# Kernel optimization log

Hardware: AMD Instinct MI355X
Metric: run time of the kernel (lower is better)

The kernel has to match this reference:

```python
import jax, jax.numpy as jnp
import numpy as np

B, M, C = 8, 8192, 256   # batch, seeds, seed feature dim
F = 128                  # vote feature dim
P, K = 256, 32           # proposals, samples per group
CA, NCLS = 256, 10       # aggregated feat dim, classes
RADIUS = 0.3


def _lin(x, w, b):
    # 1x1 conv == pointwise linear; w: (out, in)
    return jnp.einsum('...c,oc->...o', x, w) + b


def _bnrelu(x, s, t):
    # eval-mode BatchNorm folded to per-channel affine, then ReLU
    return jnp.maximum(x * s + t, 0.0)


def _fps(xyz, npoint):
    # farthest point sampling; deterministic start at index 0
    Bb, N, _ = xyz.shape
    bidx = jnp.arange(Bb)

    def step(carry, _):
        distance, farthest = carry
        centroid = xyz[bidx, farthest][:, None, :]          # (B,1,2)
        d = jnp.sum((xyz - centroid) ** 2, -1)              # (B,N)
        distance = jnp.minimum(distance, d)
        return (distance, jnp.argmax(distance, -1)), farthest

    init = (jnp.full((Bb, N), 1e10, xyz.dtype), jnp.zeros((Bb,), jnp.int32))
    _, idx = jax.lax.scan(step, init, None, length=npoint)
    return jnp.transpose(idx)                               # (B, npoint)


def _ball_query(xyz, new_xyz, radius, nsample):
    # squared-distance cdist (monotone in euclid dist, so same sort order)
    N = xyz.shape[1]
    d2 = (jnp.sum(new_xyz ** 2, -1)[:, :, None]
          + jnp.sum(xyz ** 2, -1)[:, None, :]
          - 2.0 * jnp.einsum('bsd,bnd->bsn', new_xyz, xyz))  # (B,S,N)
    gidx = jnp.broadcast_to(jnp.arange(N), d2.shape)
    # out-of-radius points replaced by group_first (= index 0, as in source)
    gidx = jnp.where(d2 > radius * radius, 0, gidx)
    order = jnp.argsort(d2, axis=-1)
    return jnp.take_along_axis(gidx, order, axis=-1)[:, :, :nsample]


def _gather(points, idx):
    # points: (B,N,C); idx: (B,...) -> (B,...,C)
    return jax.vmap(lambda p, i: p[i])(points, idx)


def _forward(seed_xyz, seed_feats,
             v_off_w1, v_off_b1, v_off_s1, v_off_t1, v_off_w2, v_off_b2,
             v_ft_w1, v_ft_b1, v_ft_s1, v_ft_t1, v_ft_w2, v_ft_b2,
             a_w1, a_b1, a_s1, a_t1, a_w2, a_b2, a_s2, a_t2,
             p_w1, p_b1, p_s1, p_t1, p_w2, p_b2, p_s2, p_t2,
             obj_w, obj_b, cls_w, cls_b):
    # --- VotingModule (vote_factor=1) ---
    h = _bnrelu(_lin(seed_feats, v_off_w1, v_off_b1), v_off_s1, v_off_t1)
    offsets = _lin(h, v_off_w2, v_off_b2)                   # (B,M,2)
    g = _bnrelu(_lin(seed_feats, v_ft_w1, v_ft_b1), v_ft_s1, v_ft_t1)
    vote_feats = _lin(g, v_ft_w2, v_ft_b2)                  # (B,M,F)
    votes_xyz = seed_xyz + offsets                          # (B,M,2)

    # --- VoteAggregation ---
    fps_idx = _fps(votes_xyz, P)                            # (B,P)
    new_xyz = _gather(votes_xyz, fps_idx)                   # (B,P,2)
    gidx = _ball_query(votes_xyz, new_xyz, RADIUS, K)       # (B,P,K)
    gv = _gather(votes_xyz, gidx)                           # (B,P,K,2)
    gf = _gather(vote_feats, gidx)                          # (B,P,K,F)
    comb = jnp.concatenate([gv - new_xyz[:, :, None, :], gf], -1)  # (B,P,K,F+2)
    x = _bnrelu(_lin(comb, a_w1, a_b1), a_s1, a_t1)
    x = _bnrelu(_lin(x, a_w2, a_b2), a_s2, a_t2)
    pooled = jnp.max(x, axis=2)                             # (B,P,CA)

    # --- ProposalHead ---
    y = _bnrelu(_lin(pooled, p_w1, p_b1), p_s1, p_t1)
    y = _bnrelu(_lin(y, p_w2, p_b2), p_s2, p_t2)
    obj = _lin(y, obj_w, obj_b)[..., 0]                     # (B,P)
    cls = _lin(y, cls_w, cls_b)                             # (B,P,NCLS)
    return (new_xyz, obj, cls)


def setup_inputs() -> dict:
    key = jax.random.key(0)
    keys = iter(jax.random.split(key, 40))

    def w(shape):
        return (jax.random.normal(next(keys), shape) * 0.05).astype(jnp.float32)

    inp = {
        'seed_xyz': jax.random.uniform(next(keys), (B, M, 2), jnp.float32),
        'seed_feats': jax.random.normal(next(keys), (B, M, C), jnp.float32),
        # voting: offset branch
        'v_off_w1': w((C, C)), 'v_off_b1': w((C,)),
        'v_off_s1': 1.0 + w((C,)), 'v_off_t1': w((C,)),
        'v_off_w2': w((2, C)), 'v_off_b2': w((2,)),
        # voting: feature branch
        'v_ft_w1': w((C, C)), 'v_ft_b1': w((C,)),
        'v_ft_s1': 1.0 + w((C,)), 'v_ft_t1': w((C,)),
        'v_ft_w2': w((F, C)), 'v_ft_b2': w((F,)),
        # aggregation MLP
        'a_w1': w((CA, F + 2)), 'a_b1': w((CA,)),
        'a_s1': 1.0 + w((CA,)), 'a_t1': w((CA,)),
        'a_w2': w((CA, CA)), 'a_b2': w((CA,)),
        'a_s2': 1.0 + w((CA,)), 'a_t2': w((CA,)),
        # proposal head
        'p_w1': w((CA, CA)), 'p_b1': w((CA,)),
        'p_s1': 1.0 + w((CA,)), 'p_t1': w((CA,)),
        'p_w2': w((CA // 2, CA)), 'p_b2': w((CA // 2,)),
        'p_s2': 1.0 + w((CA // 2,)), 'p_t2': w((CA // 2,)),
        'obj_w': w((1, CA // 2)), 'obj_b': w((1,)),
        'cls_w': w((NCLS, CA // 2)), 'cls_b': w((NCLS,)),
    }
    return inp


def reference(seed_xyz, seed_feats,
              v_off_w1, v_off_b1, v_off_s1, v_off_t1, v_off_w2, v_off_b2,
              v_ft_w1, v_ft_b1, v_ft_s1, v_ft_t1, v_ft_w2, v_ft_b2,
              a_w1, a_b1, a_s1, a_t1, a_w2, a_b2, a_s2, a_t2,
              p_w1, p_b1, p_s1, p_t1, p_w2, p_b2, p_s2, p_t2,
              obj_w, obj_b, cls_w, cls_b):
    return _forward(seed_xyz, seed_feats,
                    v_off_w1, v_off_b1, v_off_s1, v_off_t1, v_off_w2, v_off_b2,
                    v_ft_w1, v_ft_b1, v_ft_s1, v_ft_t1, v_ft_w2, v_ft_b2,
                    a_w1, a_b1, a_s1, a_t1, a_w2, a_b2, a_s2, a_t2,
                    p_w1, p_b1, p_s1, p_t1, p_w2, p_b2, p_s2, p_t2,
                    obj_w, obj_b, cls_w, cls_b)
```

## Files before the change

### kernel.cpp

```cpp
#include <hip/hip_runtime.h>

typedef __attribute__((ext_vector_type(8))) short bf16x8;
typedef __attribute__((ext_vector_type(4))) float f32x4;
typedef unsigned short u16;
typedef unsigned int u32;
typedef unsigned long long u64;

#define DEV static __device__ __forceinline__
DEV u16 f2bf(float f) { u32 i = __float_as_uint(f); i += 0x7fffu + ((i >> 16) & 1u); return (u16)(i >> 16); }
DEV float bf2f(u16 u) { return __uint_as_float(((u32)u) << 16); }

constexpr int Mn = 8192;
constexpr int Pn = 256;
constexpr int Kn = 32;
constexpr float R2 = 0.09f;

__global__ __launch_bounds__(256, 2) void k_voting_off(
    const float* __restrict__ sxyz,
    const float* __restrict__ sfeat,
    const float* __restrict__ ow1, const float* __restrict__ ob1,
    const float* __restrict__ os1, const float* __restrict__ ot1,
    const float* __restrict__ ow2, const float* __restrict__ ob2,
    float* __restrict__ votes)
{
  __shared__ __align__(16) float Xc[16][34];
  __shared__ __align__(16) float Wc[16][262];
  __shared__ __align__(16) float Hst[256][33];

  const int tid = threadIdx.x;
  const int row0 = blockIdx.x * 32;

  const int wv = tid >> 6;
  const int w8 = wv * 8;
  const int cg = tid & 63;

  float acc[8][4];
#pragma unroll
  for (int r = 0; r < 8; ++r)
#pragma unroll
    for (int j = 0; j < 4; ++j) acc[r][j] = 0.f;

  for (int kc = 0; kc < 16; ++kc) {
    __syncthreads();
    for (int i = tid; i < 256 * 16; i += 256) {
      int o = i >> 4, k = i & 15;
      Wc[k][o] = ow1[o * 256 + kc * 16 + k];
    }
    for (int i = tid; i < 32 * 16; i += 256) {
      int r = i >> 4, k = i & 15;
      Xc[k][r] = sfeat[(row0 + r) * 256 + kc * 16 + k];
    }
    __syncthreads();
#pragma unroll
    for (int k = 0; k < 16; ++k) {
      float2 x01 = *(const float2*)&Xc[k][w8];
      float2 x23 = *(const float2*)&Xc[k][w8 + 2];
      float2 x45 = *(const float2*)&Xc[k][w8 + 4];
      float2 x67 = *(const float2*)&Xc[k][w8 + 6];
      float2 wlo = *(const float2*)&Wc[k][2 * cg];
      float2 whi = *(const float2*)&Wc[k][128 + 2 * cg];
      float x[8] = {x01.x, x01.y, x23.x, x23.y, x45.x, x45.y, x67.x, x67.y};
      float w[4] = {wlo.x, wlo.y, whi.x, whi.y};
#pragma unroll
      for (int r = 0; r < 8; ++r)
#pragma unroll
        for (int j = 0; j < 4; ++j)
          acc[r][j] = fmaf(x[r], w[j], acc[r][j]);
    }
  }
  __syncthreads();
#pragma unroll
  for (int j = 0; j < 4; ++j) {
    int o = (j < 2) ? (2 * cg + j) : (126 + 2 * cg + j);
    float bb = ob1[o], ss = os1[o], tt = ot1[o];
#pragma unroll
    for (int r = 0; r < 8; ++r)
      Hst[o][w8 + r] = fmaxf((acc[r][j] + bb) * ss + tt, 0.f);
  }
  __syncthreads();

  if (tid < 64) {
    int r = tid >> 1, o = tid & 1;
    float a = 0.f;
    for (int k = 0; k < 256; ++k)
      a = fmaf(Hst[k][r], ow2[o * 256 + k], a);
    a += ob2[o];
    int row = row0 + r;
    votes[row * 2 + o] = sxyz[row * 2 + o] + a;
  }
}

__global__ __launch_bounds__(512, 1) void k_fps(
    const float* __restrict__ votes, float* __restrict__ nxyz,
    float* __restrict__ out)
{
  const int b = blockIdx.x, tid = threadIdx.x;
  const float* vb = votes + b * Mn * 2;
  __shared__ float2 xy[Mn];
  __shared__ u32 Sd[2][32], Sl[2][32];
  __shared__ float histx[256], histy[256];

  {
    const float4* vb4 = (const float4*)vb;
#pragma unroll
    for (int j = tid; j < Mn / 2; j += 512) {
      float4 v = vb4[j];
      *(float4*)&xy[2 * j] = v;
    }
  }
  float dist[16];
#pragma unroll
  for (int s = 0; s < 16; ++s) dist[s] = 1e10f;
  __syncthreads();

  float cx = xy[0].x, cy = xy[0].y;
  if (tid == 0) { histx[0] = cx; histy[0] = cy; }

  for (int it = 1; it < Pn; ++it) {
    float bd = -1.f; int sb = 0;
#pragma unroll
    for (int s = 0; s < 16; ++s) {
      float2 p = xy[s * 512 + tid];
      float dx = p.x - cx, dy = p.y - cy;
      float d = fminf(dist[s], dx * dx + dy * dy);
      dist[s] = d;
      if (d > bd) { bd = d; sb = s; }
    }
    int bi = sb * 512 + tid;

    u32 hd = __float_as_uint(bd), hl = ~(u32)bi;

#define FPS_ROR(VD, VL, N)                                                      \
    {                                                                           \
      u32 od = (u32)__builtin_amdgcn_update_dpp(0, (int)VD, 0x120 + N, 0xF, 0xF, false); \
      u32 ol = (u32)__builtin_amdgcn_update_dpp(0, (int)VL, 0x120 + N, 0xF, 0xF, false); \
      bool g = (od > VD) || (od == VD && ol > VL);                              \
      VD = g ? od : VD; VL = g ? ol : VL;                                       \
    }
    FPS_ROR(hd, hl, 8)
    FPS_ROR(hd, hl, 4)
    FPS_ROR(hd, hl, 2)
    FPS_ROR(hd, hl, 1)

    const int buf = it & 1;
    if ((tid & 15) == 0) {
      int row = tid >> 4;
      Sd[buf][row] = hd; Sl[buf][row] = hl;
    }
    __syncthreads();

    int rr = tid & 15;
    u32 rd = Sd[buf][rr], rl = Sl[buf][rr];
    {
      u32 od = Sd[buf][16 + rr], ol = Sl[buf][16 + rr];
      bool g = (od > rd) || (od == rd && ol > rl);
      rd = g ? od : rd; rl = g ? ol : rl;
    }
    FPS_ROR(rd, rl, 8)
    FPS_ROR(rd, rl, 4)
    FPS_ROR(rd, rl, 2)
    FPS_ROR(rd, rl, 1)
#undef FPS_ROR

    int widx = (int)(~rl);
    float2 w = xy[widx];
    cx = w.x; cy = w.y;
    if (tid == 0) { histx[it] = cx; histy[it] = cy; }
  }
  __syncthreads();
  if (tid < 256) {
    float2 o2; o2.x = histx[tid]; o2.y = histy[tid];
    *(float2*)&nxyz[(b * Pn + tid) * 2] = o2;
    *(float2*)&out[(b * Pn + tid) * 2] = o2;
  }
}

__global__ __launch_bounds__(256) void k_ballq(
    const float* __restrict__ votes, const float* __restrict__ nxyz,
    int* __restrict__ gidx)
{
  const int bp = blockIdx.x, tid = threadIdx.x;
  const int b = bp >> 8;
  const float* vb = votes + b * Mn * 2;
  const float sx = nxyz[bp * 2], sy = nxyz[bp * 2 + 1];
  const float a = sx * sx + sy * sy;
  float d2[32];
#pragma unroll
  for (int s = 0; s < 32; ++s) {
    int i = tid * 32 + s;
    float x = vb[i * 2], y = vb[i * 2 + 1];
    d2[s] = (a + (x * x + y * y)) - 2.f * (sx * x + sy * y);
  }
  __shared__ float sd[4];
  __shared__ int si[4];
  __shared__ int swi;
  unsigned mask = 0;
  for (int kk = 0; kk < Kn; ++kk) {
    float bd = 3.4e38f; int bi = 0x7fffffff;
#pragma unroll
    for (int s = 0; s < 32; ++s)
      if (!((mask >> s) & 1u) && d2[s] < bd) { bd = d2[s]; bi = tid * 32 + s; }
#pragma unroll
    for (int off = 32; off > 0; off >>= 1) {
      float od = __shfl_xor(bd, off);
      int oi = __shfl_xor(bi, off);
      if (od < bd || (od == bd && oi < bi)) { bd = od; bi = oi; }
    }
    if ((tid & 63) == 0) { sd[tid >> 6] = bd; si[tid >> 6] = bi; }
    __syncthreads();
    if (tid == 0) {
#pragma unroll
      for (int w = 1; w < 4; ++w)
        if (sd[w] < bd || (sd[w] == bd && si[w] < bi)) { bd = sd[w]; bi = si[w]; }
      swi = bi;
      gidx[bp * Kn + kk] = (bd > R2) ? 0 : bi;
    }
    __syncthreads();
    int wi = swi;
    if ((wi >> 5) == tid) mask |= 1u << (wi & 31);
  }
}

__global__ __launch_bounds__(256) void k_prep(
    const float* __restrict__ fw1, const float* __restrict__ fw2,
    const float* __restrict__ aw1, const float* __restrict__ aw2,
    u16* __restrict__ FW1h, u16* __restrict__ FW2b,
    u16* __restrict__ AW1b, u16* __restrict__ AW2b)
{
  const int gid = blockIdx.x * 256 + threadIdx.x;
  const int gsz = gridDim.x * 256;
  for (int i = gid; i < 65536; i += gsz) FW1h[i] = f2bf(fw1[i]);
  for (int i = gid; i < 32768; i += gsz) FW2b[i] = f2bf(fw2[i]);
  for (int i = gid; i < 65536; i += gsz) AW2b[i] = f2bf(aw2[i]);
  for (int i = gid; i < 49152; i += gsz) {
    int o = i / 192, k = i % 192;
    AW1b[i] = (k < 130) ? f2bf(aw1[o * 130 + k]) : (u16)0;
  }
}

__global__ __launch_bounds__(256) void k_vf(
    const float* __restrict__ sfeat, const u16* __restrict__ FW1h,
    const float* __restrict__ fb1, const float* __restrict__ fs1,
    const float* __restrict__ ft1, const u16* __restrict__ FW2b,
    const float* __restrict__ fb2, u16* __restrict__ vfeat)
{
  __shared__ u16 Hs[128 * 136];
  __shared__ u16 As[128 * 40];
  __shared__ u16 Bs[128 * 40];
  const int tid = threadIdx.x;
  const int row0 = blockIdx.x * 128;
  const int wid = tid >> 6, lane = tid & 63, m16 = lane & 15, quad = lane >> 4;
  const int wr = wid >> 1, wc = wid & 1;
  const int sr = tid >> 1, sk = (tid & 1) * 16;

  f32x4 acc2[4][4];
#pragma unroll
  for (int mt = 0; mt < 4; ++mt)
#pragma unroll
    for (int nt = 0; nt < 4; ++nt) acc2[mt][nt] = (f32x4){0.f, 0.f, 0.f, 0.f};

  for (int h = 0; h < 2; ++h) {
    f32x4 acc[4][4];
#pragma unroll
    for (int mt = 0; mt < 4; ++mt)
#pragma unroll
      for (int nt = 0; nt < 4; ++nt) acc[mt][nt] = (f32x4){0.f, 0.f, 0.f, 0.f};

    for (int s = 0; s < 8; ++s) {
      __syncthreads();
      {
        const float* src = &sfeat[(row0 + sr) * 256 + s * 32 + sk];
        u32 packed[8];
#pragma unroll
        for (int q = 0; q < 4; ++q) {
          float4 v = *(const float4*)&src[q * 4];
          packed[q * 2]     = (u32)f2bf(v.x) | ((u32)f2bf(v.y) << 16);
          packed[q * 2 + 1] = (u32)f2bf(v.z) | ((u32)f2bf(v.w) << 16);
        }
        *(uint4*)&As[sr * 40 + sk]     = *(uint4*)&packed[0];
        *(uint4*)&As[sr * 40 + sk + 8] = *(uint4*)&packed[4];
        const u16* bsrc = &FW1h[(h * 128 + sr) * 256 + s * 32 + sk];
        *(uint4*)&Bs[sr * 40 + sk]     = *(const uint4*)&bsrc[0];
        *(uint4*)&Bs[sr * 40 + sk + 8] = *(const uint4*)&bsrc[8];
      }
      __syncthreads();
#pragma unroll
      for (int mt = 0; mt < 4; ++mt) {
        bf16x8 af = *(const bf16x8*)&As[(wr * 64 + mt * 16 + m16) * 40 + quad * 8];
#pragma unroll
        for (int nt = 0; nt < 4; ++nt) {
          bf16x8 bfr = *(const bf16x8*)&Bs[(wc * 64 + nt * 16 + m16) * 40 + quad * 8];
          acc[mt][nt] = __builtin_amdgcn_mfma_f32_16x16x32_bf16(af, bfr, acc[mt][nt], 0, 0, 0);
        }
      }
    }
    __syncthreads();
#pragma unroll
    for (int nt = 0; nt < 4; ++nt) {
      int colL = wc * 64 + nt * 16 + m16;
      int col = h * 128 + colL;
      float bb = fb1[col], ss = fs1[col], tt = ft1[col];
#pragma unroll
      for (int mt = 0; mt < 4; ++mt) {
        int rL = wr * 64 + mt * 16 + quad * 4;
#pragma unroll
        for (int r = 0; r < 4; ++r)
          Hs[(rL + r) * 136 + colL] = f2bf(fmaxf((acc[mt][nt][r] + bb) * ss + tt, 0.f));
      }
    }
    for (int s2 = 0; s2 < 4; ++s2) {
      __syncthreads();
      {
        const u16* bsrc = &FW2b[sr * 256 + h * 128 + s2 * 32 + sk];
        *(uint4*)&Bs[sr * 40 + sk]     = *(const uint4*)&bsrc[0];
        *(uint4*)&Bs[sr * 40 + sk + 8] = *(const uint4*)&bsrc[8];
      }
      __syncthreads();
#pragma unroll
      for (int mt = 0; mt < 4; ++mt) {
        bf16x8 af = *(const bf16x8*)&Hs[(wr * 64 + mt * 16 + m16) * 136 + s2 * 32 + quad * 8];
#pragma unroll
        for (int nt = 0; nt < 4; ++nt) {
          bf16x8 bfr = *(const bf16x8*)&Bs[(wc * 64 + nt * 16 + m16) * 40 + quad * 8];
          acc2[mt][nt] = __builtin_amdgcn_mfma_f32_16x16x32_bf16(af, bfr, acc2[mt][nt], 0, 0, 0);
        }
      }
    }
  }
#pragma unroll
  for (int nt = 0; nt < 4; ++nt) {
    int col = wc * 64 + nt * 16 + m16;
    float bb = fb2[col];
#pragma unroll
    for (int mt = 0; mt < 4; ++mt) {
      int rbase = row0 + wr * 64 + mt * 16 + quad * 4;
#pragma unroll
      for (int r = 0; r < 4; ++r)
        vfeat[(rbase + r) * 128 + col] = f2bf(acc2[mt][nt][r] + bb);
    }
  }
}

__global__ __launch_bounds__(256) void k_agg(
    const float* __restrict__ votes, const u16* __restrict__ vfeat,
    const float* __restrict__ nxyz, const int* __restrict__ gidx,
    const u16* __restrict__ AW1b, const float* __restrict__ ab1,
    const float* __restrict__ as1, const float* __restrict__ at1,
    const u16* __restrict__ AW2b, const float* __restrict__ ab2,
    const float* __restrict__ as2, const float* __restrict__ at2,
    float* __restrict__ pooled)
{
  __shared__ u16 U[32 * 264];
  __shared__ u16 Bs[256 * 72];
  __shared__ int gix[32];
  __shared__ float gvx[32], gvy[32];
  u16* CombA = U;
  u16* As = U;
  float* x2T = (float*)Bs;

  const int bp = blockIdx.x, tid = threadIdx.x, b = bp >> 8;
  if (tid < 32) {
    int g = gidx[bp * 32 + tid];
    gix[tid] = g;
    gvx[tid] = votes[(b * Mn + g) * 2];
    gvy[tid] = votes[(b * Mn + g) * 2 + 1];
  }
  __syncthreads();
  const float sx = nxyz[bp * 2], sy = nxyz[bp * 2 + 1];

  if (tid < 192) {
    int row = tid / 6, c = tid % 6;
    const u16* vsrc = &vfeat[(b * Mn + gix[row]) * 128];
    u16* dst = &CombA[row * 200 + c * 32];
    if (c == 0) {
      dst[0] = f2bf(gvx[row] - sx);
      dst[1] = f2bf(gvy[row] - sy);
      for (int k = 2; k < 32; ++k) dst[k] = vsrc[k - 2];
    } else if (c <= 3) {
      for (int k = 0; k < 32; ++k) dst[k] = vsrc[c * 32 + k - 2];
    } else if (c == 4) {
      dst[0] = vsrc[126]; dst[1] = vsrc[127];
      for (int k = 2; k < 32; ++k) dst[k] = 0;
    } else {
      for (int k = 0; k < 32; ++k) dst[k] = 0;
    }
  }

  const int wid = tid >> 6, lane = tid & 63, m16 = lane & 15, quad = lane >> 4;
  const int mt = wid & 1, nh = wid >> 1;

  f32x4 acc[8];
#pragma unroll
  for (int nt = 0; nt < 8; ++nt) acc[nt] = (f32x4){0.f, 0.f, 0.f, 0.f};
  for (int s = 0; s < 3; ++s) {
    __syncthreads();
    for (int i = tid; i < 4096; i += 256) {
      int n = i >> 4, c4 = i & 15;
      *(uint2*)&Bs[n * 72 + c4 * 4] = *(const uint2*)&AW1b[n * 192 + s * 64 + c4 * 4];
    }
    __syncthreads();
#pragma unroll
    for (int ks = 0; ks < 2; ++ks) {
      bf16x8 af = *(const bf16x8*)&CombA[(mt * 16 + m16) * 200 + s * 64 + ks * 32 + quad * 8];
#pragma unroll
      for (int nt = 0; nt < 8; ++nt) {
        bf16x8 bf_ = *(const bf16x8*)&Bs[(nh * 128 + nt * 16 + m16) * 72 + ks * 32 + quad * 8];
        acc[nt] = __builtin_amdgcn_mfma_f32_16x16x32_bf16(af, bf_, acc[nt], 0, 0, 0);
      }
    }
  }
  __syncthreads();
#pragma unroll
  for (int nt = 0; nt < 8; ++nt) {
    int col = nh * 128 + nt * 16 + m16;
    float bb = ab1[col], ss = as1[col], tt = at1[col];
#pragma unroll
    for (int r = 0; r < 4; ++r) {
      int samp = mt * 16 + quad * 4 + r;
      As[samp * 264 + col] = f2bf(fmaxf((acc[nt][r] + bb) * ss + tt, 0.f));
    }
  }

  f32x4 acc2[8];
#pragma unroll
  for (int nt = 0; nt < 8; ++nt) acc2[nt] = (f32x4){0.f, 0.f, 0.f, 0.f};
  for (int s = 0; s < 4; ++s) {
    __syncthreads();
    for (int i = tid; i < 4096; i += 256) {
      int n = i >> 4, c4 = i & 15;
      *(uint2*)&Bs[n * 72 + c4 * 4] = *(const uint2*)&AW2b[n * 256 + s * 64 + c4 * 4];
    }
    __syncthreads();
#pragma unroll
    for (int ks = 0; ks < 2; ++ks) {
      bf16x8 af = *(const bf16x8*)&As[(mt * 16 + m16) * 264 + s * 64 + ks * 32 + quad * 8];
#pragma unroll
      for (int nt = 0; nt < 8; ++nt) {
        bf16x8 bf_ = *(const bf16x8*)&Bs[(nh * 128 + nt * 16 + m16) * 72 + ks * 32 + quad * 8];
        acc2[nt] = __builtin_amdgcn_mfma_f32_16x16x32_bf16(af, bf_, acc2[nt], 0, 0, 0);
      }
    }
  }
  __syncthreads();
#pragma unroll
  for (int nt = 0; nt < 8; ++nt) {
    int col = nh * 128 + nt * 16 + m16;
    float bb = ab2[col], ss = as2[col], tt = at2[col];
#pragma unroll
    for (int r = 0; r < 4; ++r) {
      int samp = mt * 16 + quad * 4 + r;
      x2T[col * 33 + samp] = fmaxf((acc2[nt][r] + bb) * ss + tt, 0.f);
    }
  }
  __syncthreads();
  {
    float m = x2T[tid * 33];
#pragma unroll
    for (int s2 = 1; s2 < 32; ++s2) m = fmaxf(m, x2T[tid * 33 + s2]);
    pooled[bp * 256 + tid] = m;
  }
}

__global__ __launch_bounds__(256) void k_head(
    const float* __restrict__ pooled,
    const float* __restrict__ pw1, const float* __restrict__ pb1,
    const float* __restrict__ ps1, const float* __restrict__ pt1,
    const float* __restrict__ pw2, const float* __restrict__ pb2,
    const float* __restrict__ ps2, const float* __restrict__ pt2,
    const float* __restrict__ objw, const float* __restrict__ objb,
    const float* __restrict__ clsw, const float* __restrict__ clsb,
    float* __restrict__ out)
{
  __shared__ float xr[256], y1[256], y2[128];
  const int bp = blockIdx.x, tid = threadIdx.x;
  xr[tid] = pooled[bp * 256 + tid];
  __syncthreads();
  {
    float a = 0.f;
    for (int c = 0; c < 256; ++c) a = fmaf(xr[c], pw1[tid * 256 + c], a);
    a = (a + pb1[tid]) * ps1[tid] + pt1[tid];
    y1[tid] = fmaxf(a, 0.f);
  }
  __syncthreads();
  if (tid < 128) {
    float a = 0.f;
    for (int c = 0; c < 256; ++c) a = fmaf(y1[c], pw2[tid * 256 + c], a);
    a = (a + pb2[tid]) * ps2[tid] + pt2[tid];
    y2[tid] = fmaxf(a, 0.f);
  }
  __syncthreads();
  if (tid < 10) {
    float a = 0.f;
    for (int c = 0; c < 128; ++c) a = fmaf(y2[c], clsw[tid * 128 + c], a);
    out[6144 + bp * 10 + tid] = a + clsb[tid];
  } else if (tid == 10) {
    float a = 0.f;
    for (int c = 0; c < 128; ++c) a = fmaf(y2[c], objw[c], a);
    out[4096 + bp] = a + objb[0];
  }
}

extern "C" void kernel_launch(void* const* d_in, const int* in_sizes, int n_in,
                              void* d_out, int out_size, void* d_ws, size_t ws_size,
                              hipStream_t stream)
{
  (void)in_sizes; (void)n_in; (void)out_size; (void)ws_size;
  const float* sxyz  = (const float*)d_in[0];
  const float* sfeat = (const float*)d_in[1];
  const float* ow1 = (const float*)d_in[2];
  const float* ob1 = (const float*)d_in[3];
  const float* os1 = (const float*)d_in[4];
  const float* ot1 = (const float*)d_in[5];
  const float* ow2 = (const float*)d_in[6];
  const float* ob2 = (const float*)d_in[7];
  const float* fw1 = (const float*)d_in[8];
  const float* fb1 = (const float*)d_in[9];
  const float* fs1 = (const float*)d_in[10];
  const float* ft1 = (const float*)d_in[11];
  const float* fw2 = (const float*)d_in[12];
  const float* fb2 = (const float*)d_in[13];
  const float* aw1 = (const float*)d_in[14];
  const float* ab1 = (const float*)d_in[15];
  const float* as1 = (const float*)d_in[16];
  const float* at1 = (const float*)d_in[17];
  const float* aw2 = (const float*)d_in[18];
  const float* ab2 = (const float*)d_in[19];
  const float* as2 = (const float*)d_in[20];
  const float* at2 = (const float*)d_in[21];
  const float* pw1 = (const float*)d_in[22];
  const float* pb1 = (const float*)d_in[23];
  const float* ps1 = (const float*)d_in[24];
  const float* pt1 = (const float*)d_in[25];
  const float* pw2 = (const float*)d_in[26];
  const float* pb2 = (const float*)d_in[27];
  const float* ps2 = (const float*)d_in[28];
  const float* pt2 = (const float*)d_in[29];
  const float* objw = (const float*)d_in[30];
  const float* objb = (const float*)d_in[31];
  const float* clsw = (const float*)d_in[32];
  const float* clsb = (const float*)d_in[33];

  char* ws = (char*)d_ws;
  float* votes  = (float*)(ws + 0);
  u16*   vfeat  = (u16*)  (ws + 524288);
  float* nxyz   = (float*)(ws + 17301504);
  int*   gidxp  = (int*)  (ws + 17317888);
  float* pooled = (float*)(ws + 17580032);
  u16*   FW1h   = (u16*)  (ws + 19677184);
  u16*   FW2b   = (u16*)  (ws + 19808256);
  u16*   AW1b   = (u16*)  (ws + 19873792);
  u16*   AW2b   = (u16*)  (ws + 19972096);
  float* out    = (float*)d_out;

  k_voting_off<<<dim3(2048), dim3(256), 0, stream>>>(
      sxyz, sfeat, ow1, ob1, os1, ot1, ow2, ob2, votes);

  k_fps<<<dim3(8), dim3(512), 0, stream>>>(votes, nxyz, out);

  k_ballq<<<dim3(2048), dim3(256), 0, stream>>>(votes, nxyz, gidxp);

  k_prep<<<dim3(256), dim3(256), 0, stream>>>(
      fw1, fw2, aw1, aw2, FW1h, FW2b, AW1b, AW2b);

  k_vf<<<dim3(512), dim3(256), 0, stream>>>(
      sfeat, FW1h, fb1, fs1, ft1, FW2b, fb2, vfeat);

  k_agg<<<dim3(2048), dim3(256), 0, stream>>>(
      votes, vfeat, nxyz, gidxp, AW1b, ab1, as1, at1,
      AW2b, ab2, as2, at2, pooled);

  k_head<<<dim3(2048), dim3(256), 0, stream>>>(
      pooled, pw1, pb1, ps1, pt1, pw2, pb2, ps2, pt2,
      objw, objb, clsw, clsb, out);
}
```

Baseline: 938.2 us.

## Merge FPS and vote-feature MLP into one launch so they overlap

Combines the serial 8-block FPS kernel and the vote-feature GEMM kernel into a single 520-block launch. The first 8 blocks run FPS and the rest run the feature MLP, so the long latency-bound FPS runs alongside the GEMM work instead of leaving most CUs idle. The GEMM part is retiled for 512 threads (8 waves, 32 columns each), and k_prep is moved ahead so its weights are ready. Risks: the shared-memory union is 86 KB and the launch bound changes, which may limit occupancy for the GEMM blocks. The FPS blocks may also be scheduled after GEMM blocks, which would stretch the critical path.

```diff
diff --git a/kernel.cpp b/kernel.cpp
--- a/kernel.cpp
+++ b/kernel.cpp
@@ -90,88 +90,194 @@
   }
 }
 
-__global__ __launch_bounds__(512, 1) void k_fps(
+__global__ __launch_bounds__(512) void k_fps_vf(
     const float* __restrict__ votes, float* __restrict__ nxyz,
-    float* __restrict__ out)
-{
-  const int b = blockIdx.x, tid = threadIdx.x;
-  const float* vb = votes + b * Mn * 2;
-  __shared__ float2 xy[Mn];
-  __shared__ u32 Sd[2][32], Sl[2][32];
-  __shared__ float histx[256], histy[256];
-
-  {
-    const float4* vb4 = (const float4*)vb;
-#pragma unroll
-    for (int j = tid; j < Mn / 2; j += 512) {
-      float4 v = vb4[j];
-      *(float4*)&xy[2 * j] = v;
-    }
-  }
-  float dist[16];
-#pragma unroll
-  for (int s = 0; s < 16; ++s) dist[s] = 1e10f;
-  __syncthreads();
-
-  float cx = xy[0].x, cy = xy[0].y;
-  if (tid == 0) { histx[0] = cx; histy[0] = cy; }
-
-  for (int it = 1; it < Pn; ++it) {
-    float bd = -1.f; int sb = 0;
-#pragma unroll
-    for (int s = 0; s < 16; ++s) {
-      float2 p = xy[s * 512 + tid];
-      float dx = p.x - cx, dy = p.y - cy;
-      float d = fminf(dist[s], dx * dx + dy * dy);
-      dist[s] = d;
-      if (d > bd) { bd = d; sb = s; }
-    }
-    int bi = sb * 512 + tid;
-
-    u32 hd = __float_as_uint(bd), hl = ~(u32)bi;
+    float* __restrict__ out,
+    const float* __restrict__ sfeat, const u16* __restrict__ FW1h,
+    const float* __restrict__ fb1, const float* __restrict__ fs1,
+    const float* __restrict__ ft1, const u16* __restrict__ FW2b,
+    const float* __restrict__ fb2, u16* __restrict__ vfeat)
+{
+  __shared__ __align__(16) char smem[86016];
+  const int tid = threadIdx.x;
+
+  if (blockIdx.x < 8) {
+    const int b = blockIdx.x;
+    const float* vb = votes + b * Mn * 2;
+    float2* xy   = (float2*)smem;
+    u32*   Sd    = (u32*)(smem + 65536);
+    u32*   Sl    = (u32*)(smem + 65536 + 256);
+    float* histx = (float*)(smem + 66048);
+    float* histy = (float*)(smem + 67072);
+
+    {
+      const float4* vb4 = (const float4*)vb;
+#pragma unroll
+      for (int j = tid; j < Mn / 2; j += 512) {
+        float4 v = vb4[j];
+        *(float4*)&xy[2 * j] = v;
+      }
+    }
+    float dist[16];
+#pragma unroll
+    for (int s = 0; s < 16; ++s) dist[s] = 1e10f;
+    __syncthreads();
+
+    float cx = xy[0].x, cy = xy[0].y;
+    if (tid == 0) { histx[0] = cx; histy[0] = cy; }
+
+    for (int it = 1; it < Pn; ++it) {
+      float bd = -1.f; int sb = 0;
+#pragma unroll
+      for (int s = 0; s < 16; ++s) {
+        float2 p = xy[s * 512 + tid];
+        float dx = p.x - cx, dy = p.y - cy;
+        float d = fminf(dist[s], dx * dx + dy * dy);
+        dist[s] = d;
+        if (d > bd) { bd = d; sb = s; }
+      }
+      int bi = sb * 512 + tid;
+
+      u32 hd = __float_as_uint(bd), hl = ~(u32)bi;
 
 #define FPS_ROR(VD, VL, N)                                                      \
-    {                                                                           \
-      u32 od = (u32)__builtin_amdgcn_update_dpp(0, (int)VD, 0x120 + N, 0xF, 0xF, false); \
-      u32 ol = (u32)__builtin_amdgcn_update_dpp(0, (int)VL, 0x120 + N, 0xF, 0xF, false); \
-      bool g = (od > VD) || (od == VD && ol > VL);                              \
-      VD = g ? od : VD; VL = g ? ol : VL;                                       \
-    }
-    FPS_ROR(hd, hl, 8)
-    FPS_ROR(hd, hl, 4)
-    FPS_ROR(hd, hl, 2)
-    FPS_ROR(hd, hl, 1)
-
-    const int buf = it & 1;
-    if ((tid & 15) == 0) {
-      int row = tid >> 4;
-      Sd[buf][row] = hd; Sl[buf][row] = hl;
-    }
-    __syncthreads();
-
-    int rr = tid & 15;
-    u32 rd = Sd[buf][rr], rl = Sl[buf][rr];
-    {
-      u32 od = Sd[buf][16 + rr], ol = Sl[buf][16 + rr];
-      bool g = (od > rd) || (od == rd && ol > rl);
-      rd = g ? od : rd; rl = g ? ol : rl;
-    }
-    FPS_ROR(rd, rl, 8)
-    FPS_ROR(rd, rl, 4)
-    FPS_ROR(rd, rl, 2)
-    FPS_ROR(rd, rl, 1)
+      {                                                                         \
+        u32 od = (u32)__builtin_amdgcn_update_dpp(0, (int)VD, 0x120 + N, 0xF, 0xF, false); \
+        u32 ol = (u32)__builtin_amdgcn_update_dpp(0, (int)VL, 0x120 + N, 0xF, 0xF, false); \
+        bool g = (od > VD) || (od == VD && ol > VL);                            \
+        VD = g ? od : VD; VL = g ? ol : VL;                                     \
+      }
+      FPS_ROR(hd, hl, 8)
+      FPS_ROR(hd, hl, 4)
+      FPS_ROR(hd, hl, 2)
+      FPS_ROR(hd, hl, 1)
+
+      const int buf = it & 1;
+      if ((tid & 15) == 0) {
+        int row = tid >> 4;
+        Sd[buf * 32 + row] = hd; Sl[buf * 32 + row] = hl;
+      }
+      __syncthreads();
+
+      int rr = tid & 15;
+      u32 rd = Sd[buf * 32 + rr], rl = Sl[buf * 32 + rr];
+      {
+        u32 od = Sd[buf * 32 + 16 + rr], ol = Sl[buf * 32 + 16 + rr];
+        bool g = (od > rd) || (od == rd && ol > rl);
+        rd = g ? od : rd; rl = g ? ol : rl;
+      }
+      FPS_ROR(rd, rl, 8)
+      FPS_ROR(rd, rl, 4)
+      FPS_ROR(rd, rl, 2)
+      FPS_ROR(rd, rl, 1)
 #undef FPS_ROR
 
-    int widx = (int)(~rl);
-    float2 w = xy[widx];
-    cx = w.x; cy = w.y;
-    if (tid == 0) { histx[it] = cx; histy[it] = cy; }
-  }
-  __syncthreads();
-  if (tid < 256) {
-    float2 o2; o2.x = histx[tid]; o2.y = histy[tid];
-    *(float2*)&nxyz[(b * Pn + tid) * 2] = o2;
-    *(float2*)&out[(b * Pn + tid) * 2] = o2;
+      int widx = (int)(~rl);
+      float2 w = xy[widx];
+      cx = w.x; cy = w.y;
+      if (tid == 0) { histx[it] = cx; histy[it] = cy; }
+    }
+    __syncthreads();
+    if (tid < 256) {
+      float2 o2; o2.x = histx[tid]; o2.y = histy[tid];
+      *(float2*)&nxyz[(b * Pn + tid) * 2] = o2;
+      *(float2*)&out[(b * Pn + tid) * 2] = o2;
+    }
+  } else {
+    const int bx = blockIdx.x - 8;
+    const int row0 = bx * 128;
+    u16* Hs = (u16*)smem;
+    u16* As = (u16*)(smem + 34816);
+    u16* Bs = (u16*)(smem + 45056);
+
+    const int wid = tid >> 6, lane = tid & 63, m16 = lane & 15, quad = lane >> 4;
+    const int wr = wid >> 2;
+    const int wc4 = wid & 3;
+    const int sr = tid >> 2, sk = (tid & 3) * 8;
+
+    f32x4 acc2[4][2];
+#pragma unroll
+    for (int mt = 0; mt < 4; ++mt)
+#pragma unroll
+      for (int nt = 0; nt < 2; ++nt) acc2[mt][nt] = (f32x4){0.f, 0.f, 0.f, 0.f};
+
+    for (int h = 0; h < 2; ++h) {
+      f32x4 acc[4][2];
+#pragma unroll
+      for (int mt = 0; mt < 4; ++mt)
+#pragma unroll
+        for (int nt = 0; nt < 2; ++nt) acc[mt][nt] = (f32x4){0.f, 0.f, 0.f, 0.f};
+
+      for (int s = 0; s < 8; ++s) {
+        __syncthreads();
+        {
+          const float* src = &sfeat[(row0 + sr) * 256 + s * 32 + sk];
+          float4 v0 = *(const float4*)&src[0];
+          float4 v1 = *(const float4*)&src[4];
+          u32 packed[4];
+          packed[0] = (u32)f2bf(v0.x) | ((u32)f2bf(v0.y) << 16);
+          packed[1] = (u32)f2bf(v0.z) | ((u32)f2bf(v0.w) << 16);
+          packed[2] = (u32)f2bf(v1.x) | ((u32)f2bf(v1.y) << 16);
+          packed[3] = (u32)f2bf(v1.z) | ((u32)f2bf(v1.w) << 16);
+          *(uint4*)&As[sr * 40 + sk] = *(uint4*)&packed[0];
+          *(uint4*)&Bs[sr * 40 + sk] =
+              *(const uint4*)&FW1h[(h * 128 + sr) * 256 + s * 32 + sk];
+        }
+        __syncthreads();
+#pragma unroll
+        for (int mt = 0; mt < 4; ++mt) {
+          bf16x8 af = *(const bf16x8*)&As[(wr * 64 + mt * 16 + m16) * 40 + quad * 8];
+#pragma unroll
+          for (int nt = 0; nt < 2; ++nt) {
+            bf16x8 bfr = *(const bf16x8*)&Bs[(wc4 * 32 + nt * 16 + m16) * 40 + quad * 8];
+            acc[mt][nt] = __builtin_amdgcn_mfma_f32_16x16x32_bf16(af, bfr, acc[mt][nt], 0, 0, 0);
+          }
+        }
+      }
+      __syncthreads();
+#pragma unroll
+      for (int nt = 0; nt < 2; ++nt) {
+        int colL = wc4 * 32 + nt * 16 + m16;
+        int col = h * 128 + colL;
+        float bb = fb1[col], ss = fs1[col], tt = ft1[col];
+#pragma unroll
+        for (int mt = 0; mt < 4; ++mt) {
+          int rL = wr * 64 + mt * 16 + quad * 4;
+#pragma unroll
+          for (int r = 0; r < 4; ++r)
+            Hs[(rL + r) * 136 + colL] = f2bf(fmaxf((acc[mt][nt][r] + bb) * ss + tt, 0.f));
+        }
+      }
+      for (int s2 = 0; s2 < 4; ++s2) {
+        __syncthreads();
+        {
+          *(uint4*)&Bs[sr * 40 + sk] =
+              *(const uint4*)&FW2b[sr * 256 + h * 128 + s2 * 32 + sk];
+        }
+        __syncthreads();
+#pragma unroll
+        for (int mt = 0; mt < 4; ++mt) {
+          bf16x8 af = *(const bf16x8*)&Hs[(wr * 64 + mt * 16 + m16) * 136 + s2 * 32 + quad * 8];
+#pragma unroll
+          for (int nt = 0; nt < 2; ++nt) {
+            bf16x8 bfr = *(const bf16x8*)&Bs[(wc4 * 32 + nt * 16 + m16) * 40 + quad * 8];
+            acc2[mt][nt] = __builtin_amdgcn_mfma_f32_16x16x32_bf16(af, bfr, acc2[mt][nt], 0, 0, 0);
+          }
+        }
+      }
+    }
+#pragma unroll
+    for (int nt = 0; nt < 2; ++nt) {
+      int col = wc4 * 32 + nt * 16 + m16;
+      float bb = fb2[col];
+#pragma unroll
+      for (int mt = 0; mt < 4; ++mt) {
+        int rbase = row0 + wr * 64 + mt * 16 + quad * 4;
+#pragma unroll
+        for (int r = 0; r < 4; ++r)
+          vfeat[(rbase + r) * 128 + col] = f2bf(acc2[mt][nt][r] + bb);
+      }
+    }
   }
 }
 
@@ -235,109 +341,6 @@
   for (int i = gid; i < 49152; i += gsz) {
     int o = i / 192, k = i % 192;
     AW1b[i] = (k < 130) ? f2bf(aw1[o * 130 + k]) : (u16)0;
-  }
-}
-
-__global__ __launch_bounds__(256) void k_vf(
-    const float* __restrict__ sfeat, const u16* __restrict__ FW1h,
-    const float* __restrict__ fb1, const float* __restrict__ fs1,
-    const float* __restrict__ ft1, const u16* __restrict__ FW2b,
-    const float* __restrict__ fb2, u16* __restrict__ vfeat)
-{
-  __shared__ u16 Hs[128 * 136];
-  __shared__ u16 As[128 * 40];
-  __shared__ u16 Bs[128 * 40];
-  const int tid = threadIdx.x;
-  const int row0 = blockIdx.x * 128;
-  const int wid = tid >> 6, lane = tid & 63, m16 = lane & 15, quad = lane >> 4;
-  const int wr = wid >> 1, wc = wid & 1;
-  const int sr = tid >> 1, sk = (tid & 1) * 16;
-
-  f32x4 acc2[4][4];
-#pragma unroll
-  for (int mt = 0; mt < 4; ++mt)
-#pragma unroll
-    for (int nt = 0; nt < 4; ++nt) acc2[mt][nt] = (f32x4){0.f, 0.f, 0.f, 0.f};
-
-  for (int h = 0; h < 2; ++h) {
-    f32x4 acc[4][4];
-#pragma unroll
-    for (int mt = 0; mt < 4; ++mt)
-#pragma unroll
-      for (int nt = 0; nt < 4; ++nt) acc[mt][nt] = (f32x4){0.f, 0.f, 0.f, 0.f};
-
-    for (int s = 0; s < 8; ++s) {
-      __syncthreads();
-      {
-        const float* src = &sfeat[(row0 + sr) * 256 + s * 32 + sk];
-        u32 packed[8];
-#pragma unroll
-        for (int q = 0; q < 4; ++q) {
-          float4 v = *(const float4*)&src[q * 4];
-          packed[q * 2]     = (u32)f2bf(v.x) | ((u32)f2bf(v.y) << 16);
-          packed[q * 2 + 1] = (u32)f2bf(v.z) | ((u32)f2bf(v.w) << 16);
-        }
-        *(uint4*)&As[sr * 40 + sk]     = *(uint4*)&packed[0];
-        *(uint4*)&As[sr * 40 + sk + 8] = *(uint4*)&packed[4];
-        const u16* bsrc = &FW1h[(h * 128 + sr) * 256 + s * 32 + sk];
-        *(uint4*)&Bs[sr * 40 + sk]     = *(const uint4*)&bsrc[0];
-        *(uint4*)&Bs[sr * 40 + sk + 8] = *(const uint4*)&bsrc[8];
-      }
-      __syncthreads();
-#pragma unroll
-      for (int mt = 0; mt < 4; ++mt) {
-        bf16x8 af = *(const bf16x8*)&As[(wr * 64 + mt * 16 + m16) * 40 + quad * 8];
-#pragma unroll
-        for (int nt = 0; nt < 4; ++nt) {
-          bf16x8 bfr = *(const bf16x8*)&Bs[(wc * 64 + nt * 16 + m16) * 40 + quad * 8];
-          acc[mt][nt] = __builtin_amdgcn_mfma_f32_16x16x32_bf16(af, bfr, acc[mt][nt], 0, 0, 0);
-        }
-      }
-    }
-    __syncthreads();
-#pragma unroll
-    for (int nt = 0; nt < 4; ++nt) {
-      int colL = wc * 64 + nt * 16 + m16;
-      int col = h * 128 + colL;
-      float bb = fb1[col], ss = fs1[col], tt = ft1[col];
-#pragma unroll
-      for (int mt = 0; mt < 4; ++mt) {
-        int rL = wr * 64 + mt * 16 + quad * 4;
-#pragma unroll
-        for (int r = 0; r < 4; ++r)
-          Hs[(rL + r) * 136 + colL] = f2bf(fmaxf((acc[mt][nt][r] + bb) * ss + tt, 0.f));
-      }
-    }
-    for (int s2 = 0; s2 < 4; ++s2) {
-      __syncthreads();
-      {
-        const u16* bsrc = &FW2b[sr * 256 + h * 128 + s2 * 32 + sk];
-        *(uint4*)&Bs[sr * 40 + sk]     = *(const uint4*)&bsrc[0];
-        *(uint4*)&Bs[sr * 40 + sk + 8] = *(const uint4*)&bsrc[8];
-      }
-      __syncthreads();
-#pragma unroll
-      for (int mt = 0; mt < 4; ++mt) {
-        bf16x8 af = *(const bf16x8*)&Hs[(wr * 64 + mt * 16 + m16) * 136 + s2 * 32 + quad * 8];
-#pragma unroll
-        for (int nt = 0; nt < 4; ++nt) {
-          bf16x8 bfr = *(const bf16x8*)&Bs[(wc * 64 + nt * 16 + m16) * 40 + quad * 8];
-          acc2[mt][nt] = __builtin_amdgcn_mfma_f32_16x16x32_bf16(af, bfr, acc2[mt][nt], 0, 0, 0);
-        }
-      }
-    }
-  }
-#pragma unroll
-  for (int nt = 0; nt < 4; ++nt) {
-    int col = wc * 64 + nt * 16 + m16;
-    float bb = fb2[col];
-#pragma unroll
-    for (int mt = 0; mt < 4; ++mt) {
-      int rbase = row0 + wr * 64 + mt * 16 + quad * 4;
-#pragma unroll
-      for (int r = 0; r < 4; ++r)
-        vfeat[(rbase + r) * 128 + col] = f2bf(acc2[mt][nt][r] + bb);
-    }
   }
 }
 
@@ -552,18 +555,17 @@
   u16*   AW2b   = (u16*)  (ws + 19972096);
   float* out    = (float*)d_out;
 
+  k_prep<<<dim3(256), dim3(256), 0, stream>>>(
+      fw1, fw2, aw1, aw2, FW1h, FW2b, AW1b, AW2b);
+
   k_voting_off<<<dim3(2048), dim3(256), 0, stream>>>(
       sxyz, sfeat, ow1, ob1, os1, ot1, ow2, ob2, votes);
 
-  k_fps<<<dim3(8), dim3(512), 0, stream>>>(votes, nxyz, out);
+  k_fps_vf<<<dim3(520), dim3(512), 0, stream>>>(
+      votes, nxyz, out,
+      sfeat, FW1h, fb1, fs1, ft1, FW2b, fb2, vfeat);
 
   k_ballq<<<dim3(2048), dim3(256), 0, stream>>>(votes, nxyz, gidxp);
-
-  k_prep<<<dim3(256), dim3(256), 0, stream>>>(
-      fw1, fw2, aw1, aw2, FW1h, FW2b, AW1b, AW2b);
-
-  k_vf<<<dim3(512), dim3(256), 0, stream>>>(
-      sfeat, FW1h, fb1, fs1, ft1, FW2b, fb2, vfeat);
 
   k_agg<<<dim3(2048), dim3(256), 0, stream>>>(
       votes, vfeat, nxyz, gidxp, AW1b, ab1, as1, at1,
```

Result: faster. 891.1 us (-5.0%).
